# Kernel tuning notes

Hardware: AMD Instinct MI355X
Metric: run time of the kernel (lower is better)

Reference implementation:

```python
import jax, jax.numpy as jnp
import numpy as np

B, S, DIM = 2, 2048, 2048
H = 16
Q_LORA, KV_LORA = 512, 512
D_NOPE, D_ROPE, D_V = 128, 64, 128
D_QK = D_NOPE + D_ROPE  # 192
SCALE = D_QK ** -0.5
EPS = 1e-6


def rmsnorm(x, w):
    return x * jax.lax.rsqrt(jnp.mean(x * x, axis=-1, keepdims=True) + EPS) * w


def apply_rope(x, cos, sin):
    # x: [B, S, h, d] with d even; cos/sin: [S, d//2] (complex-pair rotation)
    xs = x.reshape(*x.shape[:-1], -1, 2)
    x0, x1 = xs[..., 0], xs[..., 1]
    c = cos[None, :, None, :]
    s = sin[None, :, None, :]
    out = jnp.stack([x0 * c - x1 * s, x0 * s + x1 * c], axis=-1)
    return out.reshape(x.shape)


def setup_inputs() -> dict:
    key = jax.random.key(0)
    ks = jax.random.split(key, 8)
    std = 0.02
    x = jax.random.normal(ks[0], (B, S, DIM), dtype=jnp.float32)
    wq_a_w = jax.random.normal(ks[1], (DIM, Q_LORA), dtype=jnp.float32) * std
    wq_a_b = jnp.zeros((Q_LORA,), dtype=jnp.float32)
    q_norm_w = jnp.ones((Q_LORA,), dtype=jnp.float32)
    wq_b_w = jax.random.normal(ks[2], (Q_LORA, H * D_QK), dtype=jnp.float32) * std
    wkv_a_w = jax.random.normal(ks[3], (DIM, KV_LORA + D_ROPE), dtype=jnp.float32) * std
    wkv_a_b = jnp.zeros((KV_LORA + D_ROPE,), dtype=jnp.float32)
    kv_norm_w = jnp.ones((KV_LORA,), dtype=jnp.float32)
    wkv_b_w = jax.random.normal(ks[4], (KV_LORA, H * (D_NOPE + D_V)), dtype=jnp.float32) * std
    wo_w = jax.random.normal(ks[5], (H * D_V, DIM), dtype=jnp.float32) * std
    # rotary table: freqs_cis[t, i] = exp(1j * t * 10000^{-2i/d})
    inv_freq = 1.0 / (10000.0 ** (np.arange(0, D_ROPE, 2, dtype=np.float32) / D_ROPE))
    t = np.arange(S, dtype=np.float32)
    ang = np.outer(t, inv_freq)  # [S, D_ROPE//2]
    freqs_cos = jnp.asarray(np.cos(ang), dtype=jnp.float32)
    freqs_sin = jnp.asarray(np.sin(ang), dtype=jnp.float32)
    # causal mask (prefill): 0 on/below diagonal, -1e9 above
    mask = jnp.where(jnp.arange(S)[:, None] >= jnp.arange(S)[None, :], 0.0, -1e9).astype(jnp.float32)
    return {"x": x, "wq_a_w": wq_a_w, "wq_a_b": wq_a_b, "q_norm_w": q_norm_w,
            "wq_b_w": wq_b_w, "wkv_a_w": wkv_a_w, "wkv_a_b": wkv_a_b,
            "kv_norm_w": kv_norm_w, "wkv_b_w": wkv_b_w, "wo_w": wo_w,
            "freqs_cos": freqs_cos, "freqs_sin": freqs_sin, "mask": mask,
            "start_pos": 0}


def reference(x, wq_a_w, wq_a_b, q_norm_w, wq_b_w, wkv_a_w, wkv_a_b,
              kv_norm_w, wkv_b_w, wo_w, freqs_cos, freqs_sin, mask, start_pos):
    bsz, seqlen, _ = x.shape
    # low-rank Q: wq_b(q_norm(wq_a(x)))
    q = rmsnorm(x @ wq_a_w + wq_a_b, q_norm_w) @ wq_b_w
    q = q.reshape(bsz, seqlen, H, D_QK)
    q_nope, q_pe = q[..., :D_NOPE], q[..., D_NOPE:]
    q_pe = apply_rope(q_pe, freqs_cos, freqs_sin)
    # low-rank KV
    kv_full = x @ wkv_a_w + wkv_a_b
    kv, k_pe = kv_full[..., :KV_LORA], kv_full[..., KV_LORA:]
    k_pe = apply_rope(k_pe[:, :, None, :], freqs_cos, freqs_sin)  # [B,S,1,D_ROPE]
    kv = rmsnorm(kv, kv_norm_w) @ wkv_b_w
    kv = kv.reshape(bsz, seqlen, H, D_NOPE + D_V)
    k_nope, v = kv[..., :D_NOPE], kv[..., D_NOPE:]
    k = jnp.concatenate([k_nope, jnp.broadcast_to(k_pe, (bsz, seqlen, H, D_ROPE))], axis=-1)
    # prefill (start_pos=0): cache[:, :end_pos] == freshly written k, v
    q = jnp.concatenate([q_nope, q_pe], axis=-1)
    scores = jnp.einsum('bshd,bthd->bsht', q, k) * SCALE
    scores = scores + mask[None, :, None, :]
    attn = jax.nn.softmax(scores.astype(jnp.float32), axis=-1).astype(q.dtype)
    out = jnp.einsum('bsht,bthd->bshd', attn, v)
    return out.reshape(bsz, seqlen, H * D_V) @ wo_w
```

## Files before the change

kernel.cpp:

```cpp
#include <hip/hip_runtime.h>
#include <hip/hip_bf16.h>

typedef unsigned short u16;
typedef unsigned int u32;
typedef __attribute__((ext_vector_type(8))) __bf16 bf16x8;
typedef __attribute__((ext_vector_type(4))) float f32x4;
typedef __attribute__((ext_vector_type(4))) u32 u32x4;
typedef __attribute__((ext_vector_type(2))) u32 u32x2;

#define S_LEN 2048
#define BF16_ONE 0x3F80u

__device__ __forceinline__ float b2f(u16 u) {
  union { unsigned u; float f; } v; v.u = ((unsigned)u) << 16; return v.f;
}
__device__ __forceinline__ u16 f2b(float f) {
  union { float f; unsigned u; } v; v.f = f;
  unsigned r = v.u + 0x7fffu + ((v.u >> 16) & 1u);
  return (u16)(r >> 16);
}
__device__ __forceinline__ u32 cvt_pk_bf16(float a, float b) {
  u32 r;
  asm("v_cvt_pk_bf16_f32 %0, %1, %2" : "=v"(r) : "v"(a), "v"(b));
  return r;
}

__device__ __forceinline__ void glds16(const u16* g, u16* l) {
  __builtin_amdgcn_global_load_lds((const __attribute__((address_space(1))) void*)g,
                                   (__attribute__((address_space(3))) void*)l, 16, 0, 0);
}

__device__ __forceinline__ bool probe_f32(const u16* p) { return p[0] != (u16)BF16_ONE; }

struct CvtDesc {
  const void* src[7];
  u16* dst[7];
  int cum[8];
};
__global__ __launch_bounds__(256) void cvt_batch(CvtDesc d, const u16* __restrict__ probe,
                                                 int total) {
  int i = blockIdx.x * 256 + threadIdx.x;
  if (i >= total) return;
  int t = 0;
#pragma unroll
  for (int k = 1; k < 7; ++k) t += (i >= d.cum[k]);
  int li = i - d.cum[t];
  if (probe_f32(probe)) {
    const float* s = (const float*)d.src[t] + (long)li * 8;
    u16 tmp[8];
#pragma unroll
    for (int j = 0; j < 8; ++j) tmp[j] = f2b(s[j]);
    *(u32x4*)(d.dst[t] + (long)li * 8) = *(const u32x4*)tmp;
  } else {
    *(u32x4*)(d.dst[t] + (long)li * 8) = ((const u32x4*)d.src[t])[li];
  }
}

struct TrDesc {
  const void* in[5];
  u16* out[5];
  int R[5], C[5];
  int tcum[6];
  float scale[5];
};
__global__ __launch_bounds__(256) void transpose_batch(TrDesc d,
                                                       const u16* __restrict__ probe) {
  __shared__ u16 tile[32][33];
  int bid = blockIdx.x;
  int t = 0;
#pragma unroll
  for (int k = 1; k < 5; ++k) t += (bid >= d.tcum[k]);
  int rem = bid - d.tcum[t];
  const int R = d.R[t], C = d.C[t];
  const int tilesX = C >> 5;
  const int bx = rem % tilesX, by = rem / tilesX;
  const int c0 = bx * 32, r0 = by * 32;
  const int tx = threadIdx.x, ty = threadIdx.y;
  const float sc = d.scale[t];
  if (probe_f32(probe)) {
    const float* inf = (const float*)d.in[t];
#pragma unroll
    for (int i = 0; i < 4; ++i)
      tile[ty + i * 8][tx] = f2b(inf[(long)(r0 + ty + i * 8) * C + c0 + tx] * sc);
  } else {
    const u16* inb = (const u16*)d.in[t];
#pragma unroll
    for (int i = 0; i < 4; ++i)
      tile[ty + i * 8][tx] = f2b(b2f(inb[(long)(r0 + ty + i * 8) * C + c0 + tx]) * sc);
  }
  __syncthreads();
  u16* outp = d.out[t];
#pragma unroll
  for (int i = 0; i < 4; ++i)
    outp[(long)(c0 + ty + i * 8) * R + r0 + tx] = tile[tx][ty + i * 8];
}

__global__ __launch_bounds__(256) void transpose_v(const u16* __restrict__ kvb,
                                                   u16* __restrict__ vt) {
  __shared__ u16 tile[32][33];
  int s0 = blockIdx.x * 32, d0 = blockIdx.y * 32, bh = blockIdx.z;
  int b = bh >> 4, h = bh & 15;
  int tx = threadIdx.x, ty = threadIdx.y;
#pragma unroll
  for (int i = 0; i < 4; ++i)
    tile[ty + i * 8][tx] =
        kvb[((long)b * S_LEN + s0 + ty + i * 8) * 4096 + h * 256 + 128 + d0 + tx];
  __syncthreads();
#pragma unroll
  for (int i = 0; i < 4; ++i)
    vt[((long)bh * 128 + d0 + ty + i * 8) * S_LEN + s0 + tx] = tile[tx][ty + i * 8];
}

template <int MT>
__global__ __launch_bounds__(256) void gemm_bt(const u16* __restrict__ A,
                                               const u16* __restrict__ Bt,
                                               const u16* __restrict__ bias,
                                               void* __restrict__ Cv,
                                               int M, int N, int K,
                                               const u16* __restrict__ oprobe) {
  constexpr int MI = MT / 32;
  __shared__ u16 As[2][MT * 32];
  __shared__ u16 Bs[2][128 * 32];
  const int tid = threadIdx.x;
  const int lane = tid & 63;
  const int w = tid >> 6;
  const int quad = lane >> 4;
  const int l16 = lane & 15;
  const int m0 = blockIdx.y * MT;
  const int n0 = blockIdx.x * 128;
  const int wm = (w >> 1) * (MT / 2);
  const int wn = (w & 1) * 64;

  const f32x4 zero = {0.f, 0.f, 0.f, 0.f};
  f32x4 acc[MI][4];
#pragma unroll
  for (int i = 0; i < MI; ++i)
#pragma unroll
    for (int j = 0; j < 4; ++j) acc[i][j] = zero;

  auto stage = [&](int k0, int buf) {
#pragma unroll
    for (int cc = 0; cc < MT * 4; cc += 256) {
      int j = cc + tid, ar = j >> 2, ak = ((j & 3) ^ (ar & 3)) * 8;
      glds16(A + (long)(m0 + ar) * K + k0 + ak, As[buf] + j * 8);
    }
#pragma unroll
    for (int cc = 0; cc < 512; cc += 256) {
      int j = cc + tid, br = j >> 2, bk = ((j & 3) ^ (br & 3)) * 8;
      int bn = n0 + br; if (bn > N - 1) bn = N - 1;
      glds16(Bt + (long)bn * K + k0 + bk, Bs[buf] + j * 8);
    }
  };

  const int nk = K >> 5;
  stage(0, 0);
  for (int t = 0; t < nk; ++t) {
    __syncthreads();
    if (t + 1 < nk) stage((t + 1) << 5, (t + 1) & 1);
    const u16* as = As[t & 1];
    const u16* bs = Bs[t & 1];
    bf16x8 af[MI], bfr[4];
#pragma unroll
    for (int mi = 0; mi < MI; ++mi)
      af[mi] = *(const bf16x8*)(as + (wm + mi * 16 + l16) * 32 +
                                ((quad ^ (l16 & 3)) * 8));
#pragma unroll
    for (int ni = 0; ni < 4; ++ni)
      bfr[ni] = *(const bf16x8*)(bs + (wn + ni * 16 + l16) * 32 +
                                 ((quad ^ (l16 & 3)) * 8));
#pragma unroll
    for (int mi = 0; mi < MI; ++mi)
#pragma unroll
      for (int ni = 0; ni < 4; ++ni)
        acc[mi][ni] = __builtin_amdgcn_mfma_f32_16x16x32_bf16(af[mi], bfr[ni],
                                                              acc[mi][ni], 0, 0, 0);
  }

  u16* C = (u16*)Cv;
  float* Cf = (float*)Cv;
  const bool of32 = oprobe && probe_f32(oprobe);
#pragma unroll
  for (int ni = 0; ni < 4; ++ni) {
    int col = n0 + wn + ni * 16 + l16;
    if (col >= N) continue;
    float bv = bias ? b2f(bias[col]) : 0.0f;
#pragma unroll
    for (int mi = 0; mi < MI; ++mi) {
      int row = m0 + wm + mi * 16 + quad * 4;
#pragma unroll
      for (int r = 0; r < 4; ++r) {
        float val = acc[mi][ni][r] + bv;
        if (of32) Cf[(long)(row + r) * N + col] = val;
        else      C[(long)(row + r) * N + col] = f2b(val);
      }
    }
  }
}

__global__ __launch_bounds__(256) void rmsnorm512(const u16* __restrict__ in, int in_stride,
                                                  const u16* __restrict__ w,
                                                  u16* __restrict__ out, int out_stride) {
  __shared__ float red[4];
  int row = blockIdx.x, tid = threadIdx.x;
  const u16* x = in + (long)row * in_stride;
  float v0 = b2f(x[tid]), v1 = b2f(x[tid + 256]);
  float ss = v0 * v0 + v1 * v1;
#pragma unroll
  for (int off = 1; off < 64; off <<= 1) ss += __shfl_xor(ss, off);
  if ((tid & 63) == 0) red[tid >> 6] = ss;
  __syncthreads();
  float tot = red[0] + red[1] + red[2] + red[3];
  float r = rsqrtf(tot * (1.0f / 512.0f) + 1e-6f);
  u16* y = out + (long)row * out_stride;
  y[tid] = f2b(v0 * r * b2f(w[tid]));
  y[tid + 256] = f2b(v1 * r * b2f(w[tid + 256]));
}

__global__ __launch_bounds__(256) void rope_q_kernel(u16* __restrict__ q,
                                                     const u16* __restrict__ fc,
                                                     const u16* __restrict__ fs) {
  int i = blockIdx.x * 256 + threadIdx.x;
  int pair = i & 31;
  int h = (i >> 5) & 15;
  int row = i >> 9;
  int pos = row & (S_LEN - 1);
  long base = (long)row * 3072 + h * 192 + 128 + pair * 2;
  float x0 = b2f(q[base]), x1 = b2f(q[base + 1]);
  float c = b2f(fc[pos * 32 + pair]), s = b2f(fs[pos * 32 + pair]);
  q[base] = f2b(x0 * c - x1 * s);
  q[base + 1] = f2b(x0 * s + x1 * c);
}

__global__ __launch_bounds__(256) void rope_k_kernel(const u16* __restrict__ kva,
                                                     u16* __restrict__ kpe,
                                                     const u16* __restrict__ fc,
                                                     const u16* __restrict__ fs) {
  int i = blockIdx.x * 256 + threadIdx.x;
  int pair = i & 31;
  int row = i >> 5;
  int pos = row & (S_LEN - 1);
  long sb = (long)row * 576 + 512 + pair * 2;
  float x0 = b2f(kva[sb]), x1 = b2f(kva[sb + 1]);
  float c = b2f(fc[pos * 32 + pair]), s = b2f(fs[pos * 32 + pair]);
  kpe[(long)row * 64 + pair * 2] = f2b(x0 * c - x1 * s);
  kpe[(long)row * 64 + pair * 2 + 1] = f2b(x0 * s + x1 * c);
}

__global__ __launch_bounds__(512, 1) void mla_attn(const u16* __restrict__ q,
                                                   const u16* __restrict__ kvb,
                                                   const u16* __restrict__ vt,
                                                   const u16* __restrict__ kpe,
                                                   u16* __restrict__ o) {
  __shared__ u16 Ks[2][64 * 192];
  __shared__ u16 Vts[2][128 * 64];
  const int tid = threadIdx.x;
  const int w = tid >> 6;
  const int lane = tid & 63;
  const int quad = lane >> 4;
  const int l16 = lane & 15;
  const int bh = blockIdx.x;
  const int b = bh >> 4, h = bh & 15;
  const long rowbase = (long)b * S_LEN;
  const f32x4 zero = {0.f, 0.f, 0.f, 0.f};

  auto stage_k = [&](int t0s, u16* dst) {
#pragma unroll
    for (int tt = 0; tt < 3; ++tt) {
      int j = tt * 512 + tid;
      int r = j / 24, csw = j % 24;
      int c = csw ^ (r & 7);
      const u16* src = (c < 16)
                           ? (kvb + (rowbase + t0s + r) * 4096 + h * 256 + c * 8)
                           : (kpe + (rowbase + t0s + r) * 64 + (c - 16) * 8);
      glds16(src, dst + j * 8);
    }
  };
  auto stage_v = [&](int t0s, u16* dst) {
#pragma unroll
    for (int tt = 0; tt < 2; ++tt) {
      int j = tt * 512 + tid;
      int d = j >> 3, c = (j & 7) ^ (d & 7);
      glds16(vt + ((long)bh * 128 + d) * S_LEN + t0s + c * 8, dst + j * 8);
    }
  };

  const int srcA = (((quad & 1) << 1) | (quad >> 1)) * 16 + l16;
  const int srcB = srcA ^ 16;
  const bool lowq = quad < 2;
  const int p = quad & 1;

  const int yy = blockIdx.y;
  const int jt = (yy < 8) ? yy : 23 - yy;
  const int q0 = jt * 128;
  const int ntiles = 2 * jt + 2;
  const int rowlo = q0 + w * 16;

  const u16* qrow_p = q + (rowbase + rowlo + l16) * 3072 + h * 192;
  bf16x8 qf[6];
#pragma unroll
  for (int kk = 0; kk < 6; ++kk)
    qf[kk] = *(const bf16x8*)(qrow_p + kk * 32 + quad * 8);

  float m_r = -INFINITY;
  float l_r = 0.f;
  f32x4 oacc[8];
#pragma unroll
  for (int i = 0; i < 8; ++i) oacc[i] = zero;

  stage_k(0, Ks[0]);
  stage_v(0, Vts[0]);

  for (int t = 0; t < ntiles; ++t) {
    __syncthreads();
    if (t + 1 < ntiles) {
      stage_k((t + 1) * 64, Ks[(t + 1) & 1]);
      stage_v((t + 1) * 64, Vts[(t + 1) & 1]);
    }
    const int t0 = t * 64;
    if (rowlo + 15 < t0) continue;
    const u16* ks = Ks[t & 1];
    const u16* vs = Vts[t & 1];
    const bool needmask = (t0 + 63 > rowlo);

    f32x4 s[4] = {zero, zero, zero, zero};
    __builtin_amdgcn_s_setprio(1);
#pragma unroll
    for (int kk = 0; kk < 6; ++kk) {
      const int csw = ((kk * 4 + quad) ^ (l16 & 7)) * 8;
#pragma unroll
      for (int g = 0; g < 4; ++g) {
        bf16x8 kf = *(const bf16x8*)(ks + (g * 16 + l16) * 192 + csw);
        s[g] = __builtin_amdgcn_mfma_f32_16x16x32_bf16(kf, qf[kk], s[g], 0, 0, 0);
      }
    }
    __builtin_amdgcn_s_setprio(0);

    if (needmask) {
      const int lim = rowlo + l16 - t0 - quad * 4;
#pragma unroll
      for (int g = 0; g < 4; ++g)
#pragma unroll
        for (int r = 0; r < 4; ++r)
          s[g][r] = (g * 16 + r > lim) ? -1e30f : s[g][r];
    }

    float mx0 = fmaxf(fmaxf(s[0][0], s[0][1]), fmaxf(s[0][2], s[0][3]));
    float mx1 = fmaxf(fmaxf(s[1][0], s[1][1]), fmaxf(s[1][2], s[1][3]));
    float mx2 = fmaxf(fmaxf(s[2][0], s[2][1]), fmaxf(s[2][2], s[2][3]));
    float mx3 = fmaxf(fmaxf(s[3][0], s[3][1]), fmaxf(s[3][2], s[3][3]));
    float vmax = fmaxf(fmaxf(mx0, mx1), fmaxf(mx2, mx3));
    vmax = fmaxf(vmax, __shfl_xor(vmax, 16));
    vmax = fmaxf(vmax, __shfl_xor(vmax, 32));

    if (!__all(vmax <= m_r + 8.0f)) {
      float mnew = fmaxf(m_r, vmax);
      float alpha = __expf(m_r - mnew);
      m_r = mnew;
      l_r *= alpha;
      float al0 = __shfl(alpha, (lane & 48) | (quad * 4 + 0));
      float al1 = __shfl(alpha, (lane & 48) | (quad * 4 + 1));
      float al2 = __shfl(alpha, (lane & 48) | (quad * 4 + 2));
      float al3 = __shfl(alpha, (lane & 48) | (quad * 4 + 3));
#pragma unroll
      for (int nt = 0; nt < 8; ++nt) {
        f32x4 tt = oacc[nt];
        tt[0] *= al0; tt[1] *= al1; tt[2] *= al2; tt[3] *= al3;
        oacc[nt] = tt;
      }
    }

    u32 pk0x, pk0y, pk1x, pk1y, pk2x, pk2y, pk3x, pk3y;
    float sum = 0.f;
    {
      float e00 = __expf(s[0][0] - m_r), e01 = __expf(s[0][1] - m_r);
      float e02 = __expf(s[0][2] - m_r), e03 = __expf(s[0][3] - m_r);
      float e10 = __expf(s[1][0] - m_r), e11 = __expf(s[1][1] - m_r);
      float e12 = __expf(s[1][2] - m_r), e13 = __expf(s[1][3] - m_r);
      float e20 = __expf(s[2][0] - m_r), e21 = __expf(s[2][1] - m_r);
      float e22 = __expf(s[2][2] - m_r), e23 = __expf(s[2][3] - m_r);
      float e30 = __expf(s[3][0] - m_r), e31 = __expf(s[3][1] - m_r);
      float e32 = __expf(s[3][2] - m_r), e33 = __expf(s[3][3] - m_r);
      sum = ((e00 + e01) + (e02 + e03)) + ((e10 + e11) + (e12 + e13)) +
            ((e20 + e21) + (e22 + e23)) + ((e30 + e31) + (e32 + e33));
      pk0x = cvt_pk_bf16(e00, e01); pk0y = cvt_pk_bf16(e02, e03);
      pk1x = cvt_pk_bf16(e10, e11); pk1y = cvt_pk_bf16(e12, e13);
      pk2x = cvt_pk_bf16(e20, e21); pk2y = cvt_pk_bf16(e22, e23);
      pk3x = cvt_pk_bf16(e30, e31); pk3y = cvt_pk_bf16(e32, e33);
    }
    l_r += sum;

    u32 a0c = p ? pk1x : pk0x, a1c = p ? pk1y : pk0y;
    u32 a2c = p ? pk3x : pk2x, a3c = p ? pk3y : pk2y;
    u32 b0c = p ? pk0x : pk1x, b1c = p ? pk0y : pk1y;
    u32 b2c = p ? pk2x : pk3x, b3c = p ? pk2y : pk3y;
    u32 A0 = __shfl(a0c, srcA), A1 = __shfl(a1c, srcA);
    u32 A2 = __shfl(a2c, srcA), A3 = __shfl(a3c, srcA);
    u32 B0 = __shfl(b0c, srcB), B1 = __shfl(b1c, srcB);
    u32 B2 = __shfl(b2c, srcB), B3 = __shfl(b3c, srcB);
    u32x4 w0 = {lowq ? A0 : B0, lowq ? A1 : B1, lowq ? B0 : A0, lowq ? B1 : A1};
    u32x4 w1 = {lowq ? A2 : B2, lowq ? A3 : B3, lowq ? B2 : A2, lowq ? B3 : A3};
    bf16x8 ap0 = __builtin_bit_cast(bf16x8, w0);
    bf16x8 ap1 = __builtin_bit_cast(bf16x8, w1);

    __builtin_amdgcn_s_setprio(1);
#pragma unroll
    for (int nt = 0; nt < 8; ++nt) {
      bf16x8 bv0 = *(const bf16x8*)(vs + (nt * 16 + l16) * 64 +
                                    ((quad ^ (l16 & 7)) * 8));
      bf16x8 bv1 = *(const bf16x8*)(vs + (nt * 16 + l16) * 64 +
                                    (((4 + quad) ^ (l16 & 7)) * 8));
      oacc[nt] = __builtin_amdgcn_mfma_f32_16x16x32_bf16(ap0, bv0, oacc[nt], 0, 0, 0);
      oacc[nt] = __builtin_amdgcn_mfma_f32_16x16x32_bf16(ap1, bv1, oacc[nt], 0, 0, 0);
    }
    __builtin_amdgcn_s_setprio(0);
  }

  float ls = l_r;
  ls += __shfl_xor(ls, 16);
  ls += __shfl_xor(ls, 32);
  float i0 = __fdividef(1.0f, __shfl(ls, (lane & 48) | (quad * 4 + 0)));
  float i1 = __fdividef(1.0f, __shfl(ls, (lane & 48) | (quad * 4 + 1)));
  float i2 = __fdividef(1.0f, __shfl(ls, (lane & 48) | (quad * 4 + 2)));
  float i3 = __fdividef(1.0f, __shfl(ls, (lane & 48) | (quad * 4 + 3)));
  const long orow = rowbase + q0 + w * 16 + quad * 4;
#pragma unroll
  for (int nt = 0; nt < 8; ++nt) {
    o[(orow + 0) * 2048 + h * 128 + nt * 16 + l16] = f2b(oacc[nt][0] * i0);
    o[(orow + 1) * 2048 + h * 128 + nt * 16 + l16] = f2b(oacc[nt][1] * i1);
    o[(orow + 2) * 2048 + h * 128 + nt * 16 + l16] = f2b(oacc[nt][2] * i2);
    o[(orow + 3) * 2048 + h * 128 + nt * 16 + l16] = f2b(oacc[nt][3] * i3);
  }
}

extern "C" void kernel_launch(void* const* d_in, const int* in_sizes, int n_in,
                              void* d_out, int out_size, void* d_ws, size_t ws_size,
                              hipStream_t stream) {
  const void* x_raw    = d_in[0];
  const void* wqa_raw  = d_in[1];
  const void* wqab_raw = d_in[2];
  const void* qnw_raw  = d_in[3];
  const void* wqb_raw  = d_in[4];
  const void* wkva_raw = d_in[5];
  const void* wkvab_raw= d_in[6];
  const void* kvnw_raw = d_in[7];
  const void* wkvb_raw = d_in[8];
  const void* wo_raw   = d_in[9];
  const void* fc_raw   = d_in[10];
  const void* fs_raw   = d_in[11];
  const u16* probe = (const u16*)qnw_raw;
  const float SC = 0.07216878364870323f;

  char* ws = (char*)d_ws;
  size_t off = 0;
  auto alloc = [&](size_t n) { void* p = ws + off; off += (n + 255) & ~(size_t)255; return p; };
  u16* xb     = (u16*)alloc(4096ull * 2048 * 2);
  u16* fcb    = (u16*)alloc(2048ull * 32 * 2);
  u16* fsb    = (u16*)alloc(2048ull * 32 * 2);
  u16* wqab_b = (u16*)alloc(512ull * 2);
  u16* qnw_b  = (u16*)alloc(512ull * 2);
  u16* wkvab_b= (u16*)alloc(576ull * 2);
  u16* kvnw_b = (u16*)alloc(512ull * 2);
  u16* wqa_t  = (u16*)alloc(512ull * 2048 * 2);
  u16* wqb_t  = (u16*)alloc(3072ull * 512 * 2);
  u16* wkva_t = (u16*)alloc(576ull * 2048 * 2);
  u16* wkvb_t = (u16*)alloc(4096ull * 512 * 2);
  u16* wo_t   = (u16*)alloc(2048ull * 2048 * 2);
  u16* qa     = (u16*)alloc(4096ull * 512 * 2);
  u16* qbuf   = (u16*)alloc(4096ull * 3072 * 2);
  u16* kva    = (u16*)alloc(4096ull * 576 * 2);
  u16* kvn    = (u16*)alloc(4096ull * 512 * 2);
  u16* kpe    = (u16*)alloc(4096ull * 64 * 2);
  u16* kvb    = (u16*)alloc(4096ull * 4096 * 2);
  u16* vtb    = (u16*)alloc(32ull * 128 * 2048 * 2);
  u16* attn   = (u16*)alloc(4096ull * 2048 * 2);

  CvtDesc cd;
  const void* csrc[7] = {x_raw, fc_raw, fs_raw, wqab_raw, qnw_raw, wkvab_raw, kvnw_raw};
  u16* cdst[7] = {xb, fcb, fsb, wqab_b, qnw_b, wkvab_b, kvnw_b};
  long cn[7] = {4096l * 2048, 2048l * 32, 2048l * 32, 512, 512, 576, 512};
  int cum = 0;
  for (int i = 0; i < 7; ++i) {
    cd.src[i] = csrc[i]; cd.dst[i] = cdst[i];
    cd.cum[i] = cum; cum += (int)(cn[i] / 8);
  }
  cd.cum[7] = cum;
  cvt_batch<<<(cum + 255) / 256, 256, 0, stream>>>(cd, probe, cum);

  TrDesc td;
  const void* tin[5] = {wqa_raw, wqb_raw, wkva_raw, wkvb_raw, wo_raw};
  u16* tout[5] = {wqa_t, wqb_t, wkva_t, wkvb_t, wo_t};
  int tR[5] = {2048, 512, 2048, 512, 2048};
  int tC[5] = {512, 3072, 576, 4096, 2048};
  float tsc[5] = {1.0f, SC, 1.0f, 1.0f, 1.0f};
  int tcum = 0;
  for (int i = 0; i < 5; ++i) {
    td.in[i] = tin[i]; td.out[i] = tout[i];
    td.R[i] = tR[i]; td.C[i] = tC[i]; td.scale[i] = tsc[i];
    td.tcum[i] = tcum; tcum += (tR[i] / 32) * (tC[i] / 32);
  }
  td.tcum[5] = tcum;
  transpose_batch<<<tcum, dim3(32, 8), 0, stream>>>(td, probe);

  gemm_bt<64><<<dim3(4, 64), 256, 0, stream>>>(xb, wqa_t, wqab_b, qa, 4096, 512, 2048, nullptr);
  rmsnorm512<<<4096, 256, 0, stream>>>(qa, 512, qnw_b, qa, 512);
  gemm_bt<128><<<dim3(24, 32), 256, 0, stream>>>(qa, wqb_t, nullptr, qbuf, 4096, 3072, 512, nullptr);
  rope_q_kernel<<<8192, 256, 0, stream>>>(qbuf, fcb, fsb);

  gemm_bt<64><<<dim3(5, 64), 256, 0, stream>>>(xb, wkva_t, wkvab_b, kva, 4096, 576, 2048, nullptr);
  rmsnorm512<<<4096, 256, 0, stream>>>(kva, 576, kvnw_b, kvn, 512);
  rope_k_kernel<<<512, 256, 0, stream>>>(kva, kpe, fcb, fsb);
  gemm_bt<128><<<dim3(32, 32), 256, 0, stream>>>(kvn, wkvb_t, nullptr, kvb, 4096, 4096, 512, nullptr);
  transpose_v<<<dim3(64, 4, 32), dim3(32, 8), 0, stream>>>(kvb, vtb);

  mla_attn<<<dim3(32, 16), 512, 0, stream>>>(qbuf, kvb, vtb, kpe, attn);

  gemm_bt<128><<<dim3(16, 32), 256, 0, stream>>>(attn, wo_t, nullptr, d_out, 4096, 2048, 2048, probe);
}
```

Baseline: 428.6 us.

## Process two 16-row query tiles per wave in MLA attention with 256-thread blocks

The attention kernel now uses 4 waves of 256 threads instead of 8, with each wave handling 32 query rows as two 16-row halves. Each K and V fragment read from LDS feeds two MFMAs, which halves LDS reads per MFMA. V is now single-buffered and loaded within the current iteration, with an extra barrier before the PV step. Launch bounds change to (256,2) so two blocks can share a CU. The cost is higher register pressure from the doubled accumulators and Q fragments, and V loads are no longer prefetched a tile ahead.

```diff
diff --git a/kernel.cpp b/kernel.cpp
--- a/kernel.cpp
+++ b/kernel.cpp
@@ -246,13 +246,13 @@
   kpe[(long)row * 64 + pair * 2 + 1] = f2b(x0 * s + x1 * c);
 }
 
-__global__ __launch_bounds__(512, 1) void mla_attn(const u16* __restrict__ q,
+__global__ __launch_bounds__(256, 2) void mla_attn(const u16* __restrict__ q,
                                                    const u16* __restrict__ kvb,
                                                    const u16* __restrict__ vt,
                                                    const u16* __restrict__ kpe,
                                                    u16* __restrict__ o) {
   __shared__ u16 Ks[2][64 * 192];
-  __shared__ u16 Vts[2][128 * 64];
+  __shared__ u16 Vts[128 * 64];
   const int tid = threadIdx.x;
   const int w = tid >> 6;
   const int lane = tid & 63;
@@ -265,8 +265,8 @@
 
   auto stage_k = [&](int t0s, u16* dst) {
 #pragma unroll
-    for (int tt = 0; tt < 3; ++tt) {
-      int j = tt * 512 + tid;
+    for (int tt = 0; tt < 6; ++tt) {
+      int j = tt * 256 + tid;
       int r = j / 24, csw = j % 24;
       int c = csw ^ (r & 7);
       const u16* src = (c < 16)
@@ -275,12 +275,12 @@
       glds16(src, dst + j * 8);
     }
   };
-  auto stage_v = [&](int t0s, u16* dst) {
-#pragma unroll
-    for (int tt = 0; tt < 2; ++tt) {
-      int j = tt * 512 + tid;
+  auto stage_v = [&](int t0s) {
+#pragma unroll
+    for (int tt = 0; tt < 4; ++tt) {
+      int j = tt * 256 + tid;
       int d = j >> 3, c = (j & 7) ^ (d & 7);
-      glds16(vt + ((long)bh * 128 + d) * S_LEN + t0s + c * 8, dst + j * 8);
+      glds16(vt + ((long)bh * 128 + d) * S_LEN + t0s + c * 8, Vts + j * 8);
     }
   };
 
@@ -293,57 +293,32 @@
   const int jt = (yy < 8) ? yy : 23 - yy;
   const int q0 = jt * 128;
   const int ntiles = 2 * jt + 2;
-  const int rowlo = q0 + w * 16;
-
-  const u16* qrow_p = q + (rowbase + rowlo + l16) * 3072 + h * 192;
-  bf16x8 qf[6];
-#pragma unroll
-  for (int kk = 0; kk < 6; ++kk)
-    qf[kk] = *(const bf16x8*)(qrow_p + kk * 32 + quad * 8);
-
-  float m_r = -INFINITY;
-  float l_r = 0.f;
-  f32x4 oacc[8];
-#pragma unroll
-  for (int i = 0; i < 8; ++i) oacc[i] = zero;
-
-  stage_k(0, Ks[0]);
-  stage_v(0, Vts[0]);
-
-  for (int t = 0; t < ntiles; ++t) {
-    __syncthreads();
-    if (t + 1 < ntiles) {
-      stage_k((t + 1) * 64, Ks[(t + 1) & 1]);
-      stage_v((t + 1) * 64, Vts[(t + 1) & 1]);
-    }
-    const int t0 = t * 64;
-    if (rowlo + 15 < t0) continue;
-    const u16* ks = Ks[t & 1];
-    const u16* vs = Vts[t & 1];
-    const bool needmask = (t0 + 63 > rowlo);
-
-    f32x4 s[4] = {zero, zero, zero, zero};
-    __builtin_amdgcn_s_setprio(1);
-#pragma unroll
-    for (int kk = 0; kk < 6; ++kk) {
-      const int csw = ((kk * 4 + quad) ^ (l16 & 7)) * 8;
-#pragma unroll
-      for (int g = 0; g < 4; ++g) {
-        bf16x8 kf = *(const bf16x8*)(ks + (g * 16 + l16) * 192 + csw);
-        s[g] = __builtin_amdgcn_mfma_f32_16x16x32_bf16(kf, qf[kk], s[g], 0, 0, 0);
-      }
-    }
-    __builtin_amdgcn_s_setprio(0);
-
+  const int rowlo = q0 + w * 32;
+
+  const u16* qrowA = q + (rowbase + rowlo + l16) * 3072 + h * 192;
+  const u16* qrowB = qrowA + 16 * 3072;
+  bf16x8 qfA[6], qfB[6];
+#pragma unroll
+  for (int kk = 0; kk < 6; ++kk) {
+    qfA[kk] = *(const bf16x8*)(qrowA + kk * 32 + quad * 8);
+    qfB[kk] = *(const bf16x8*)(qrowB + kk * 32 + quad * 8);
+  }
+
+  float mA = -INFINITY, mB = -INFINITY;
+  float lA = 0.f, lB = 0.f;
+  f32x4 oA[8], oB[8];
+#pragma unroll
+  for (int i = 0; i < 8; ++i) { oA[i] = zero; oB[i] = zero; }
+
+  auto finish_half = [&](f32x4* s, float& m_r, float& l_r, f32x4* oacc,
+                         int lim, bool needmask, bf16x8& ap0, bf16x8& ap1) {
     if (needmask) {
-      const int lim = rowlo + l16 - t0 - quad * 4;
 #pragma unroll
       for (int g = 0; g < 4; ++g)
 #pragma unroll
         for (int r = 0; r < 4; ++r)
           s[g][r] = (g * 16 + r > lim) ? -1e30f : s[g][r];
     }
-
     float mx0 = fmaxf(fmaxf(s[0][0], s[0][1]), fmaxf(s[0][2], s[0][3]));
     float mx1 = fmaxf(fmaxf(s[1][0], s[1][1]), fmaxf(s[1][2], s[1][3]));
     float mx2 = fmaxf(fmaxf(s[2][0], s[2][1]), fmaxf(s[2][2], s[2][3]));
@@ -369,25 +344,20 @@
       }
     }
 
-    u32 pk0x, pk0y, pk1x, pk1y, pk2x, pk2y, pk3x, pk3y;
-    float sum = 0.f;
-    {
-      float e00 = __expf(s[0][0] - m_r), e01 = __expf(s[0][1] - m_r);
-      float e02 = __expf(s[0][2] - m_r), e03 = __expf(s[0][3] - m_r);
-      float e10 = __expf(s[1][0] - m_r), e11 = __expf(s[1][1] - m_r);
-      float e12 = __expf(s[1][2] - m_r), e13 = __expf(s[1][3] - m_r);
-      float e20 = __expf(s[2][0] - m_r), e21 = __expf(s[2][1] - m_r);
-      float e22 = __expf(s[2][2] - m_r), e23 = __expf(s[2][3] - m_r);
-      float e30 = __expf(s[3][0] - m_r), e31 = __expf(s[3][1] - m_r);
-      float e32 = __expf(s[3][2] - m_r), e33 = __expf(s[3][3] - m_r);
-      sum = ((e00 + e01) + (e02 + e03)) + ((e10 + e11) + (e12 + e13)) +
-            ((e20 + e21) + (e22 + e23)) + ((e30 + e31) + (e32 + e33));
-      pk0x = cvt_pk_bf16(e00, e01); pk0y = cvt_pk_bf16(e02, e03);
-      pk1x = cvt_pk_bf16(e10, e11); pk1y = cvt_pk_bf16(e12, e13);
-      pk2x = cvt_pk_bf16(e20, e21); pk2y = cvt_pk_bf16(e22, e23);
-      pk3x = cvt_pk_bf16(e30, e31); pk3y = cvt_pk_bf16(e32, e33);
-    }
-    l_r += sum;
+    float e00 = __expf(s[0][0] - m_r), e01 = __expf(s[0][1] - m_r);
+    float e02 = __expf(s[0][2] - m_r), e03 = __expf(s[0][3] - m_r);
+    float e10 = __expf(s[1][0] - m_r), e11 = __expf(s[1][1] - m_r);
+    float e12 = __expf(s[1][2] - m_r), e13 = __expf(s[1][3] - m_r);
+    float e20 = __expf(s[2][0] - m_r), e21 = __expf(s[2][1] - m_r);
+    float e22 = __expf(s[2][2] - m_r), e23 = __expf(s[2][3] - m_r);
+    float e30 = __expf(s[3][0] - m_r), e31 = __expf(s[3][1] - m_r);
+    float e32 = __expf(s[3][2] - m_r), e33 = __expf(s[3][3] - m_r);
+    l_r += ((e00 + e01) + (e02 + e03)) + ((e10 + e11) + (e12 + e13)) +
+           ((e20 + e21) + (e22 + e23)) + ((e30 + e31) + (e32 + e33));
+    u32 pk0x = cvt_pk_bf16(e00, e01), pk0y = cvt_pk_bf16(e02, e03);
+    u32 pk1x = cvt_pk_bf16(e10, e11), pk1y = cvt_pk_bf16(e12, e13);
+    u32 pk2x = cvt_pk_bf16(e20, e21), pk2y = cvt_pk_bf16(e22, e23);
+    u32 pk3x = cvt_pk_bf16(e30, e31), pk3y = cvt_pk_bf16(e32, e33);
 
     u32 a0c = p ? pk1x : pk0x, a1c = p ? pk1y : pk0y;
     u32 a2c = p ? pk3x : pk2x, a3c = p ? pk3y : pk2y;
@@ -399,37 +369,79 @@
     u32 B2 = __shfl(b2c, srcB), B3 = __shfl(b3c, srcB);
     u32x4 w0 = {lowq ? A0 : B0, lowq ? A1 : B1, lowq ? B0 : A0, lowq ? B1 : A1};
     u32x4 w1 = {lowq ? A2 : B2, lowq ? A3 : B3, lowq ? B2 : A2, lowq ? B3 : A3};
-    bf16x8 ap0 = __builtin_bit_cast(bf16x8, w0);
-    bf16x8 ap1 = __builtin_bit_cast(bf16x8, w1);
-
-    __builtin_amdgcn_s_setprio(1);
+    ap0 = __builtin_bit_cast(bf16x8, w0);
+    ap1 = __builtin_bit_cast(bf16x8, w1);
+  };
+
+  stage_k(0, Ks[0]);
+
+  for (int t = 0; t < ntiles; ++t) {
+    __syncthreads();
+    stage_v(t * 64);
+    if (t + 1 < ntiles) stage_k((t + 1) * 64, Ks[(t + 1) & 1]);
+    const int t0 = t * 64;
+    const bool active = (rowlo + 31 >= t0);
+    bf16x8 apA0, apA1, apB0, apB1;
+    if (active) {
+      const u16* ks = Ks[t & 1];
+      f32x4 sA[4] = {zero, zero, zero, zero};
+      f32x4 sB[4] = {zero, zero, zero, zero};
+      __builtin_amdgcn_s_setprio(1);
+#pragma unroll
+      for (int kk = 0; kk < 6; ++kk) {
+        const int csw = ((kk * 4 + quad) ^ (l16 & 7)) * 8;
+#pragma unroll
+        for (int g = 0; g < 4; ++g) {
+          bf16x8 kf = *(const bf16x8*)(ks + (g * 16 + l16) * 192 + csw);
+          sA[g] = __builtin_amdgcn_mfma_f32_16x16x32_bf16(kf, qfA[kk], sA[g], 0, 0, 0);
+          sB[g] = __builtin_amdgcn_mfma_f32_16x16x32_bf16(kf, qfB[kk], sB[g], 0, 0, 0);
+        }
+      }
+      __builtin_amdgcn_s_setprio(0);
+
+      const bool nmA = (t0 + 63 > rowlo);
+      const bool nmB = (t0 + 63 > rowlo + 16);
+      const int limA = rowlo + l16 - t0 - quad * 4;
+      finish_half(sA, mA, lA, oA, limA, nmA, apA0, apA1);
+      finish_half(sB, mB, lB, oB, limA + 16, nmB, apB0, apB1);
+    }
+    __syncthreads();
+    if (active) {
+      __builtin_amdgcn_s_setprio(1);
+#pragma unroll
+      for (int nt = 0; nt < 8; ++nt) {
+        bf16x8 bv0 = *(const bf16x8*)(Vts + (nt * 16 + l16) * 64 +
+                                      ((quad ^ (l16 & 7)) * 8));
+        bf16x8 bv1 = *(const bf16x8*)(Vts + (nt * 16 + l16) * 64 +
+                                      (((4 + quad) ^ (l16 & 7)) * 8));
+        oA[nt] = __builtin_amdgcn_mfma_f32_16x16x32_bf16(apA0, bv0, oA[nt], 0, 0, 0);
+        oA[nt] = __builtin_amdgcn_mfma_f32_16x16x32_bf16(apA1, bv1, oA[nt], 0, 0, 0);
+        oB[nt] = __builtin_amdgcn_mfma_f32_16x16x32_bf16(apB0, bv0, oB[nt], 0, 0, 0);
+        oB[nt] = __builtin_amdgcn_mfma_f32_16x16x32_bf16(apB1, bv1, oB[nt], 0, 0, 0);
+      }
+      __builtin_amdgcn_s_setprio(0);
+    }
+  }
+
+  auto write_half = [&](float l_r, f32x4* oacc, long orow) {
+    float ls = l_r;
+    ls += __shfl_xor(ls, 16);
+    ls += __shfl_xor(ls, 32);
+    float i0 = __fdividef(1.0f, __shfl(ls, (lane & 48) | (quad * 4 + 0)));
+    float i1 = __fdividef(1.0f, __shfl(ls, (lane & 48) | (quad * 4 + 1)));
+    float i2 = __fdividef(1.0f, __shfl(ls, (lane & 48) | (quad * 4 + 2)));
+    float i3 = __fdividef(1.0f, __shfl(ls, (lane & 48) | (quad * 4 + 3)));
 #pragma unroll
     for (int nt = 0; nt < 8; ++nt) {
-      bf16x8 bv0 = *(const bf16x8*)(vs + (nt * 16 + l16) * 64 +
-                                    ((quad ^ (l16 & 7)) * 8));
-      bf16x8 bv1 = *(const bf16x8*)(vs + (nt * 16 + l16) * 64 +
-                                    (((4 + quad) ^ (l16 & 7)) * 8));
-      oacc[nt] = __builtin_amdgcn_mfma_f32_16x16x32_bf16(ap0, bv0, oacc[nt], 0, 0, 0);
-      oacc[nt] = __builtin_amdgcn_mfma_f32_16x16x32_bf16(ap1, bv1, oacc[nt], 0, 0, 0);
-    }
-    __builtin_amdgcn_s_setprio(0);
-  }
-
-  float ls = l_r;
-  ls += __shfl_xor(ls, 16);
-  ls += __shfl_xor(ls, 32);
-  float i0 = __fdividef(1.0f, __shfl(ls, (lane & 48) | (quad * 4 + 0)));
-  float i1 = __fdividef(1.0f, __shfl(ls, (lane & 48) | (quad * 4 + 1)));
-  float i2 = __fdividef(1.0f, __shfl(ls, (lane & 48) | (quad * 4 + 2)));
-  float i3 = __fdividef(1.0f, __shfl(ls, (lane & 48) | (quad * 4 + 3)));
-  const long orow = rowbase + q0 + w * 16 + quad * 4;
-#pragma unroll
-  for (int nt = 0; nt < 8; ++nt) {
-    o[(orow + 0) * 2048 + h * 128 + nt * 16 + l16] = f2b(oacc[nt][0] * i0);
-    o[(orow + 1) * 2048 + h * 128 + nt * 16 + l16] = f2b(oacc[nt][1] * i1);
-    o[(orow + 2) * 2048 + h * 128 + nt * 16 + l16] = f2b(oacc[nt][2] * i2);
-    o[(orow + 3) * 2048 + h * 128 + nt * 16 + l16] = f2b(oacc[nt][3] * i3);
-  }
+      o[(orow + 0) * 2048 + h * 128 + nt * 16 + l16] = f2b(oacc[nt][0] * i0);
+      o[(orow + 1) * 2048 + h * 128 + nt * 16 + l16] = f2b(oacc[nt][1] * i1);
+      o[(orow + 2) * 2048 + h * 128 + nt * 16 + l16] = f2b(oacc[nt][2] * i2);
+      o[(orow + 3) * 2048 + h * 128 + nt * 16 + l16] = f2b(oacc[nt][3] * i3);
+    }
+  };
+  const long orowA = rowbase + rowlo + quad * 4;
+  write_half(lA, oA, orowA);
+  write_half(lB, oB, orowA + 16);
 }
 
 extern "C" void kernel_launch(void* const* d_in, const int* in_sizes, int n_in,
@@ -512,7 +524,7 @@
   gemm_bt<128><<<dim3(32, 32), 256, 0, stream>>>(kvn, wkvb_t, nullptr, kvb, 4096, 4096, 512, nullptr);
   transpose_v<<<dim3(64, 4, 32), dim3(32, 8), 0, stream>>>(kvb, vtb);
 
-  mla_attn<<<dim3(32, 16), 512, 0, stream>>>(qbuf, kvb, vtb, kpe, attn);
+  mla_attn<<<dim3(32, 16), 256, 0, stream>>>(qbuf, kvb, vtb, kpe, attn);
 
   gemm_bt<128><<<dim3(16, 32), 256, 0, stream>>>(attn, wo_t, nullptr, d_out, 4096, 2048, 2048, probe);
 }
```

After: 433.9 us. Within noise of the previous version (+1.3%).
